# Performance work log

Hardware: AMD Instinct MI355X
Metric: run time of the kernel (lower is better)

## Reference

```python
import jax, jax.numpy as jnp
import numpy as np

N = 50000      # nodes
E = 600000     # edges (avg degree 12)
IN, H, OUT = 128, 256, 256


def setup_inputs() -> dict:
    key = jax.random.key(0)
    ks = jax.random.split(key, 9)
    glorot = lambda k, shp: jax.random.uniform(
        k, shp, jnp.float32, -1.0, 1.0) * np.sqrt(6.0 / (shp[0] + shp[1]))
    return {
        "x": jax.random.normal(ks[0], (N, IN), jnp.float32),
        "src": jax.random.randint(ks[1], (E,), 0, N, jnp.int32),
        "dst": jax.random.randint(ks[2], (E,), 0, N, jnp.int32),
        "W_conv": glorot(ks[3], (IN, H)),
        "b_conv": jnp.zeros((H,), jnp.float32),
        "W_fc": glorot(ks[4], (H, H)),
        "b_fc": jax.random.uniform(ks[5], (H,), jnp.float32, -1, 1) / np.sqrt(H),
        "W_fc2": glorot(ks[6], (H, OUT)),
        "b_fc2": jax.random.uniform(ks[7], (OUT,), jnp.float32, -1, 1) / np.sqrt(OUT),
    }


def reference(x, src, dst, W_conv, b_conv, W_fc, b_fc, W_fc2, b_fc2):
    ones = jnp.ones((E,), x.dtype)
    # dgl GraphConv, norm='both': D_in^{-1/2} A D_out^{-1/2} X W + b
    deg_out = jax.ops.segment_sum(ones, src, num_segments=N)
    deg_in = jax.ops.segment_sum(ones, dst, num_segments=N)
    norm_src = jax.lax.rsqrt(jnp.maximum(deg_out, 1.0))  # [N]
    norm_dst = jax.lax.rsqrt(jnp.maximum(deg_in, 1.0))   # [N]
    feat = x * norm_src[:, None]                          # [N, IN]
    agg = jax.ops.segment_sum(feat[src], dst, num_segments=N)  # gather+scatter SpMM
    h = agg * norm_dst[:, None]
    h = h @ W_conv + b_conv                               # GraphConv weight+bias
    # num_nonl_layers == 2 branch
    h = jax.nn.relu(h) @ W_fc + b_fc
    h = jax.nn.relu(h) @ W_fc2 + b_fc2
    return h
```

## Files before the change

kernel.cpp:

```cpp
#include <hip/hip_runtime.h>

#define NN 50000
#define NE 600000
#define FIN 128
#define CAPS 128
#define CAPU 64
#define PW1 136
#define PW2 264

typedef __attribute__((ext_vector_type(8))) short bf16x8;
typedef __attribute__((ext_vector_type(4))) float f32x4;

__device__ __forceinline__ unsigned short f2bf(float f) {
    union { float f; unsigned int i; } v; v.f = f;
    return (unsigned short)((v.i + 0x7FFFu + ((v.i >> 16) & 1u)) >> 16);
}


__global__ __launch_bounds__(256)
void bin_kernel(const int* __restrict__ src, const int* __restrict__ dst,
                int* __restrict__ cnt_in, int* __restrict__ cnt_out,
                int* __restrict__ csr_src) {
    int e = blockIdx.x * 256 + threadIdx.x;
    if (e < NE) {
        int s = src[e], d = dst[e];
        int p = atomicAdd(&cnt_in[d], 1);
        if (p < CAPU) csr_src[d * CAPS + p] = s;
        atomicAdd(&cnt_out[s], 1);
    }
}

__global__ __launch_bounds__(256)
void gather_kernel(const float* __restrict__ x, const int* __restrict__ csr_src,
                   const int* __restrict__ cnt_in, const int* __restrict__ cnt_out,
                   char* __restrict__ slotbase) {
    int tid  = threadIdx.x;
    int grp  = tid >> 5;
    int lane = tid & 31;
    int r = blockIdx.x * 8 + grp;
    if (r >= NN) return;
    int deg = cnt_in[r];
    float nd = rsqrtf(fmaxf((float)deg, 1.0f));
    int cnt = deg > CAPU ? CAPU : deg;
    const int* bucket = csr_src + (size_t)r * CAPS;
    const float* xb = x + lane * 4;
    float4 acc = {0.f, 0.f, 0.f, 0.f};
    for (int j0 = 0; j0 < cnt; j0 += 32) {
        int c = cnt - j0; if (c > 32) c = 32;
        int sv = 0; float nsl = 0.f;
        if (lane < c) {
            sv  = bucket[j0 + lane];
            nsl = rsqrtf(fmaxf((float)cnt_out[sv], 1.0f));
        }
        int i = 0;
        for (; i + 4 <= c; i += 4) {
            int   s0 = __shfl(sv, i, 32),     s1 = __shfl(sv, i + 1, 32);
            int   s2 = __shfl(sv, i + 2, 32), s3 = __shfl(sv, i + 3, 32);
            float n0 = __shfl(nsl, i, 32),     n1 = __shfl(nsl, i + 1, 32);
            float n2 = __shfl(nsl, i + 2, 32), n3 = __shfl(nsl, i + 3, 32);
            float4 v0 = *(const float4*)(xb + (size_t)s0 * FIN);
            float4 v1 = *(const float4*)(xb + (size_t)s1 * FIN);
            float4 v2 = *(const float4*)(xb + (size_t)s2 * FIN);
            float4 v3 = *(const float4*)(xb + (size_t)s3 * FIN);
            acc.x += v0.x * n0; acc.y += v0.y * n0; acc.z += v0.z * n0; acc.w += v0.w * n0;
            acc.x += v1.x * n1; acc.y += v1.y * n1; acc.z += v1.z * n1; acc.w += v1.w * n1;
            acc.x += v2.x * n2; acc.y += v2.y * n2; acc.z += v2.z * n2; acc.w += v2.w * n2;
            acc.x += v3.x * n3; acc.y += v3.y * n3; acc.z += v3.z * n3; acc.w += v3.w * n3;
        }
        for (; i < c; ++i) {
            int   s  = __shfl(sv,  i, 32);
            float ns = __shfl(nsl, i, 32);
            float4 xv = *(const float4*)(xb + (size_t)s * FIN);
            acc.x += xv.x * ns; acc.y += xv.y * ns;
            acc.z += xv.z * ns; acc.w += xv.w * ns;
        }
    }
    unsigned short o[4];
    o[0] = f2bf(acc.x * nd); o[1] = f2bf(acc.y * nd);
    o[2] = f2bf(acc.z * nd); o[3] = f2bf(acc.w * nd);
    *(uint2*)(slotbase + (size_t)r * 1024 + 768 + lane * 8) = *(const uint2*)o;
}

__global__ __launch_bounds__(256)
void wprep_kernel(const float* __restrict__ Wc, const float* __restrict__ W1,
                  const float* __restrict__ W2, unsigned short* __restrict__ o) {
    int t = blockIdx.x * 256 + threadIdx.x;
    if (t < 32768) {
        int n = t >> 7, k = t & 127;
        o[t] = f2bf(Wc[k * 256 + n]);
    } else if (t < 98304) {
        int i = t - 32768; int n = i >> 8, k = i & 255;
        o[32768 + i] = f2bf(W1[k * 256 + n]);
    } else if (t < 163840) {
        int i = t - 98304; int n = i >> 8, k = i & 255;
        o[98304 + i] = f2bf(W2[k * 256 + n]);
    }
}

__global__ __launch_bounds__(256)
void gemm1_kernel(char* slotbase, const unsigned short* __restrict__ Wct,
                  const float* __restrict__ bc) {
    __shared__ short wsh[64 * PW1];
    int tid = threadIdx.x;
    int wave = tid >> 6, lane = tid & 63;
    int quad = lane >> 4, l16 = lane & 15;
    int m0 = blockIdx.x * 128 + wave * 32;
    bf16x8 a[2][4];
    #pragma unroll
    for (int g = 0; g < 2; ++g) {
        int arow = m0 + g * 16 + l16; if (arow >= NN) arow = NN - 1;
        const unsigned short* Ap =
            (const unsigned short*)(slotbase + (size_t)arow * 1024 + 768) + quad * 8;
        #pragma unroll
        for (int i = 0; i < 4; ++i) a[g][i] = *(const bf16x8*)(Ap + i * 32);
    }
    int sc = tid >> 2, sq = tid & 3;
    #pragma unroll 1
    for (int p = 0; p < 2; ++p) {
        int n0 = blockIdx.y * 128 + p * 64;
        __syncthreads();
        {
            const unsigned short* g = Wct + (size_t)(n0 + sc) * 128 + sq * 32;
            #pragma unroll
            for (int j = 0; j < 4; ++j)
                *(bf16x8*)&wsh[sc * PW1 + sq * 32 + j * 8] = *(const bf16x8*)(g + j * 8);
        }
        __syncthreads();
        f32x4 acc[2][4] = {};
        #pragma unroll
        for (int i = 0; i < 4; ++i) {
            int k0 = i * 32;
            bf16x8 b0 = *(const bf16x8*)&wsh[( 0 + l16) * PW1 + quad * 8 + k0];
            bf16x8 b1 = *(const bf16x8*)&wsh[(16 + l16) * PW1 + quad * 8 + k0];
            bf16x8 b2 = *(const bf16x8*)&wsh[(32 + l16) * PW1 + quad * 8 + k0];
            bf16x8 b3 = *(const bf16x8*)&wsh[(48 + l16) * PW1 + quad * 8 + k0];
            #pragma unroll
            for (int g = 0; g < 2; ++g) {
                acc[g][0] = __builtin_amdgcn_mfma_f32_16x16x32_bf16(a[g][i], b0, acc[g][0], 0, 0, 0);
                acc[g][1] = __builtin_amdgcn_mfma_f32_16x16x32_bf16(a[g][i], b1, acc[g][1], 0, 0, 0);
                acc[g][2] = __builtin_amdgcn_mfma_f32_16x16x32_bf16(a[g][i], b2, acc[g][2], 0, 0, 0);
                acc[g][3] = __builtin_amdgcn_mfma_f32_16x16x32_bf16(a[g][i], b3, acc[g][3], 0, 0, 0);
            }
        }
        #pragma unroll
        for (int c = 0; c < 4; ++c) {
            int col = n0 + c * 16 + l16;
            float bv = bc[col];
            #pragma unroll
            for (int g = 0; g < 2; ++g) {
                #pragma unroll
                for (int r2 = 0; r2 < 4; ++r2) {
                    int rr = m0 + g * 16 + quad * 4 + r2;
                    if (rr < NN)
                        *(unsigned short*)(slotbase + (size_t)rr * 1024 + 2 * col) =
                            f2bf(fmaxf(acc[g][c][r2] + bv, 0.0f));
                }
            }
        }
    }
}

__global__ __launch_bounds__(256)
void gemm2_kernel(char* slotbase, const unsigned short* __restrict__ Wt,
                  const float* __restrict__ bias) {
    __shared__ short wsh[64 * PW2];
    int tid = threadIdx.x;
    int wave = tid >> 6, lane = tid & 63;
    int quad = lane >> 4, l16 = lane & 15;
    int m0 = blockIdx.x * 128 + wave * 32;
    bf16x8 a[2][8];
    #pragma unroll
    for (int g = 0; g < 2; ++g) {
        int arow = m0 + g * 16 + l16; if (arow >= NN) arow = NN - 1;
        const unsigned short* Ap =
            (const unsigned short*)(slotbase + (size_t)arow * 1024) + quad * 8;
        #pragma unroll
        for (int i = 0; i < 8; ++i) a[g][i] = *(const bf16x8*)(Ap + i * 32);
    }
    int sc = tid >> 2, sq = tid & 3;
    #pragma unroll 1
    for (int p = 0; p < 2; ++p) {
        int n0 = blockIdx.y * 128 + p * 64;
        __syncthreads();
        {
            const unsigned short* g = Wt + (size_t)(n0 + sc) * 256 + sq * 64;
            #pragma unroll
            for (int j = 0; j < 8; ++j)
                *(bf16x8*)&wsh[sc * PW2 + sq * 64 + j * 8] = *(const bf16x8*)(g + j * 8);
        }
        __syncthreads();
        f32x4 acc[2][4] = {};
        #pragma unroll
        for (int i = 0; i < 8; ++i) {
            int k0 = i * 32;
            bf16x8 b0 = *(const bf16x8*)&wsh[( 0 + l16) * PW2 + quad * 8 + k0];
            bf16x8 b1 = *(const bf16x8*)&wsh[(16 + l16) * PW2 + quad * 8 + k0];
            bf16x8 b2 = *(const bf16x8*)&wsh[(32 + l16) * PW2 + quad * 8 + k0];
            bf16x8 b3 = *(const bf16x8*)&wsh[(48 + l16) * PW2 + quad * 8 + k0];
            #pragma unroll
            for (int g = 0; g < 2; ++g) {
                acc[g][0] = __builtin_amdgcn_mfma_f32_16x16x32_bf16(a[g][i], b0, acc[g][0], 0, 0, 0);
                acc[g][1] = __builtin_amdgcn_mfma_f32_16x16x32_bf16(a[g][i], b1, acc[g][1], 0, 0, 0);
                acc[g][2] = __builtin_amdgcn_mfma_f32_16x16x32_bf16(a[g][i], b2, acc[g][2], 0, 0, 0);
                acc[g][3] = __builtin_amdgcn_mfma_f32_16x16x32_bf16(a[g][i], b3, acc[g][3], 0, 0, 0);
            }
        }
        #pragma unroll
        for (int c = 0; c < 4; ++c) {
            int col = n0 + c * 16 + l16;
            float bv = bias[col];
            #pragma unroll
            for (int g = 0; g < 2; ++g) {
                #pragma unroll
                for (int r2 = 0; r2 < 4; ++r2) {
                    int rr = m0 + g * 16 + quad * 4 + r2;
                    if (rr < NN)
                        *(unsigned short*)(slotbase + (size_t)rr * 1024 + 512 + 2 * col) =
                            f2bf(fmaxf(acc[g][c][r2] + bv, 0.0f));
                }
            }
        }
    }
}

__global__ __launch_bounds__(256)
void gemm3_kernel(char* slotbase, const unsigned short* __restrict__ Wt,
                  const float* __restrict__ bias) {
    __shared__ short wsh[64 * PW2];
    int tid = threadIdx.x;
    int wave = tid >> 6, lane = tid & 63;
    int quad = lane >> 4, l16 = lane & 15;
    int m0 = blockIdx.x * 64 + wave * 16;
    int arow = m0 + l16; if (arow >= NN) arow = NN - 1;
    const unsigned short* Ap =
        (const unsigned short*)(slotbase + (size_t)arow * 1024 + 512) + quad * 8;
    bf16x8 a[8];
    #pragma unroll
    for (int i = 0; i < 8; ++i) a[i] = *(const bf16x8*)(Ap + i * 32);
    int sc = tid >> 2, sq = tid & 3;
    #pragma unroll 1
    for (int p = 0; p < 4; ++p) {
        __syncthreads();
        {
            const unsigned short* g = Wt + (size_t)(p * 64 + sc) * 256 + sq * 64;
            #pragma unroll
            for (int j = 0; j < 8; ++j)
                *(bf16x8*)&wsh[sc * PW2 + sq * 64 + j * 8] = *(const bf16x8*)(g + j * 8);
        }
        __syncthreads();
        f32x4 ac0 = {0.f,0.f,0.f,0.f}, ac1 = ac0, ac2 = ac0, ac3 = ac0;
        #pragma unroll
        for (int i = 0; i < 8; ++i) {
            int k0 = i * 32;
            bf16x8 b0 = *(const bf16x8*)&wsh[( 0 + l16) * PW2 + quad * 8 + k0];
            bf16x8 b1 = *(const bf16x8*)&wsh[(16 + l16) * PW2 + quad * 8 + k0];
            bf16x8 b2 = *(const bf16x8*)&wsh[(32 + l16) * PW2 + quad * 8 + k0];
            bf16x8 b3 = *(const bf16x8*)&wsh[(48 + l16) * PW2 + quad * 8 + k0];
            ac0 = __builtin_amdgcn_mfma_f32_16x16x32_bf16(a[i], b0, ac0, 0, 0, 0);
            ac1 = __builtin_amdgcn_mfma_f32_16x16x32_bf16(a[i], b1, ac1, 0, 0, 0);
            ac2 = __builtin_amdgcn_mfma_f32_16x16x32_bf16(a[i], b2, ac2, 0, 0, 0);
            ac3 = __builtin_amdgcn_mfma_f32_16x16x32_bf16(a[i], b3, ac3, 0, 0, 0);
        }
        int n0 = p * 64;
        f32x4 accs[4] = {ac0, ac1, ac2, ac3};
        #pragma unroll
        for (int c = 0; c < 4; ++c) {
            int col = n0 + c * 16 + l16;
            float bv = bias[col];
            #pragma unroll
            for (int r2 = 0; r2 < 4; ++r2) {
                int rr = m0 + quad * 4 + r2;
                if (rr < NN)
                    *(float*)(slotbase + (size_t)rr * 1024 + 4 * col) = accs[c][r2] + bv;
            }
        }
    }
}


extern "C" void kernel_launch(void* const* d_in, const int* in_sizes, int n_in,
                              void* d_out, int out_size, void* d_ws, size_t ws_size,
                              hipStream_t stream) {
    const float* x      = (const float*)d_in[0];
    const int*   src    = (const int*)d_in[1];
    const int*   dst    = (const int*)d_in[2];
    const float* W_conv = (const float*)d_in[3];
    const float* b_conv = (const float*)d_in[4];
    const float* W_fc   = (const float*)d_in[5];
    const float* b_fc   = (const float*)d_in[6];
    const float* W_fc2  = (const float*)d_in[7];
    const float* b_fc2  = (const float*)d_in[8];
    char* slotbase = (char*)d_out;

    int* csr_src = (int*)(slotbase + 16000000);

    char* ws = (char*)d_ws;
    int* cnt_out = (int*)(ws + 0);
    int* cnt_in  = (int*)(ws + 204800);
    unsigned short* Wct = (unsigned short*)(ws + 0);
    unsigned short* W1t = (unsigned short*)(ws + 65536);
    unsigned short* W2t = (unsigned short*)(ws + 196608);

    hipMemsetAsync(d_ws, 0, 409600, stream);

    bin_kernel<<<(NE + 255) / 256, 256, 0, stream>>>(src, dst, cnt_in, cnt_out,
                                                     csr_src);
    gather_kernel<<<(NN + 7) / 8, 256, 0, stream>>>(x, csr_src, cnt_in, cnt_out,
                                                    slotbase);
    wprep_kernel<<<640, 256, 0, stream>>>(W_conv, W_fc, W_fc2, (unsigned short*)ws);

    dim3 g12((NN + 127) / 128, 2);
    gemm1_kernel<<<g12, 256, 0, stream>>>(slotbase, Wct, b_conv);
    gemm2_kernel<<<g12, 256, 0, stream>>>(slotbase, W1t, b_fc);
    gemm3_kernel<<<(NN + 63) / 64, 256, 0, stream>>>(slotbase, W2t, b_fc2);
}
```

Before: 271.4 us.

## Pre-scale node features to bf16 before gather, fuse with weight prep

Adds a prep kernel that multiplies each node row by its out-degree norm and stores it as bf16 in workspace. The same launch also converts the weights to bf16. The gather then reads half the bytes per neighbour and skips the per-edge cnt_out lookup and rsqrt. The cost is an extra full pass over x, workspace use, and bf16 rounding of the inputs before accumulation; if the workspace is too small, the old fp32 path is used instead.

Result: faster. 257.0 us (-5.3%).

```diff
diff --git a/kernel.cpp b/kernel.cpp
--- a/kernel.cpp
+++ b/kernel.cpp
@@ -7,6 +7,8 @@
 #define CAPU 64
 #define PW1 136
 #define PW2 264
+#define PRE_BLOCKS 3125
+#define WP_BLOCKS  640
 
 typedef __attribute__((ext_vector_type(8))) short bf16x8;
 typedef __attribute__((ext_vector_type(4))) float f32x4;
@@ -14,6 +16,12 @@
 __device__ __forceinline__ unsigned short f2bf(float f) {
     union { float f; unsigned int i; } v; v.f = f;
     return (unsigned short)((v.i + 0x7FFFu + ((v.i >> 16) & 1u)) >> 16);
+}
+__device__ __forceinline__ float bflo(unsigned int u) {
+    union { unsigned int i; float f; } v; v.i = u << 16; return v.f;
+}
+__device__ __forceinline__ float bfhi(unsigned int u) {
+    union { unsigned int i; float f; } v; v.i = u & 0xffff0000u; return v.f;
 }
 
 
@@ -31,9 +39,87 @@
 }
 
 __global__ __launch_bounds__(256)
-void gather_kernel(const float* __restrict__ x, const int* __restrict__ csr_src,
-                   const int* __restrict__ cnt_in, const int* __restrict__ cnt_out,
+void prep_kernel(const float* __restrict__ x, const int* __restrict__ cnt_out,
+                 unsigned short* __restrict__ xn,
+                 const float* __restrict__ Wc, const float* __restrict__ W1,
+                 const float* __restrict__ W2, unsigned short* __restrict__ wout) {
+    int b = blockIdx.x;
+    if (b < PRE_BLOCKS) {
+        int idx = b * 256 + threadIdx.x;
+        int row = idx >> 4;
+        float sc = rsqrtf(fmaxf((float)cnt_out[row], 1.0f));
+        const float4* xp = (const float4*)(x + (size_t)idx * 8);
+        float4 a = xp[0], c = xp[1];
+        unsigned int w0 = f2bf(a.x * sc) | ((unsigned int)f2bf(a.y * sc) << 16);
+        unsigned int w1 = f2bf(a.z * sc) | ((unsigned int)f2bf(a.w * sc) << 16);
+        unsigned int w2 = f2bf(c.x * sc) | ((unsigned int)f2bf(c.y * sc) << 16);
+        unsigned int w3 = f2bf(c.z * sc) | ((unsigned int)f2bf(c.w * sc) << 16);
+        uint4 o = {w0, w1, w2, w3};
+        *(uint4*)(xn + (size_t)idx * 8) = o;
+    } else {
+        int t = (b - PRE_BLOCKS) * 256 + threadIdx.x;
+        if (t < 32768) {
+            int n = t >> 7, k = t & 127;
+            wout[t] = f2bf(Wc[k * 256 + n]);
+        } else if (t < 98304) {
+            int i = t - 32768; int n = i >> 8, k = i & 255;
+            wout[32768 + i] = f2bf(W1[k * 256 + n]);
+        } else if (t < 163840) {
+            int i = t - 98304; int n = i >> 8, k = i & 255;
+            wout[98304 + i] = f2bf(W2[k * 256 + n]);
+        }
+    }
+}
+
+__global__ __launch_bounds__(256)
+void gather_kernel(const unsigned short* __restrict__ xn,
+                   const int* __restrict__ csr_src,
+                   const int* __restrict__ cnt_in,
                    char* __restrict__ slotbase) {
+    int tid  = threadIdx.x;
+    int grp  = tid >> 5;
+    int lane = tid & 31;
+    int r = blockIdx.x * 8 + grp;
+    if (r >= NN) return;
+    int deg = cnt_in[r];
+    float nd = rsqrtf(fmaxf((float)deg, 1.0f));
+    int cnt = deg > CAPU ? CAPU : deg;
+    const int* bucket = csr_src + (size_t)r * CAPS;
+    const unsigned short* xb = xn + lane * 4;
+    float4 acc = {0.f, 0.f, 0.f, 0.f};
+    for (int j0 = 0; j0 < cnt; j0 += 32) {
+        int c = cnt - j0; if (c > 32) c = 32;
+        int sv = (lane < c) ? bucket[j0 + lane] : 0;
+        int i = 0;
+        for (; i + 4 <= c; i += 4) {
+            int s0 = __shfl(sv, i,     32), s1 = __shfl(sv, i + 1, 32);
+            int s2 = __shfl(sv, i + 2, 32), s3 = __shfl(sv, i + 3, 32);
+            uint2 w0 = *(const uint2*)(xb + (size_t)s0 * FIN);
+            uint2 w1 = *(const uint2*)(xb + (size_t)s1 * FIN);
+            uint2 w2 = *(const uint2*)(xb + (size_t)s2 * FIN);
+            uint2 w3 = *(const uint2*)(xb + (size_t)s3 * FIN);
+            acc.x += bflo(w0.x); acc.y += bfhi(w0.x); acc.z += bflo(w0.y); acc.w += bfhi(w0.y);
+            acc.x += bflo(w1.x); acc.y += bfhi(w1.x); acc.z += bflo(w1.y); acc.w += bfhi(w1.y);
+            acc.x += bflo(w2.x); acc.y += bfhi(w2.x); acc.z += bflo(w2.y); acc.w += bfhi(w2.y);
+            acc.x += bflo(w3.x); acc.y += bfhi(w3.x); acc.z += bflo(w3.y); acc.w += bfhi(w3.y);
+        }
+        for (; i < c; ++i) {
+            int s = __shfl(sv, i, 32);
+            uint2 w = *(const uint2*)(xb + (size_t)s * FIN);
+            acc.x += bflo(w.x); acc.y += bfhi(w.x);
+            acc.z += bflo(w.y); acc.w += bfhi(w.y);
+        }
+    }
+    unsigned short o[4];
+    o[0] = f2bf(acc.x * nd); o[1] = f2bf(acc.y * nd);
+    o[2] = f2bf(acc.z * nd); o[3] = f2bf(acc.w * nd);
+    *(uint2*)(slotbase + (size_t)r * 1024 + 768 + lane * 8) = *(const uint2*)o;
+}
+
+__global__ __launch_bounds__(256)
+void gather_fb_kernel(const float* __restrict__ x, const int* __restrict__ csr_src,
+                      const int* __restrict__ cnt_in, const int* __restrict__ cnt_out,
+                      char* __restrict__ slotbase) {
     int tid  = threadIdx.x;
     int grp  = tid >> 5;
     int lane = tid & 31;
@@ -52,22 +138,7 @@
             sv  = bucket[j0 + lane];
             nsl = rsqrtf(fmaxf((float)cnt_out[sv], 1.0f));
         }
-        int i = 0;
-        for (; i + 4 <= c; i += 4) {
-            int   s0 = __shfl(sv, i, 32),     s1 = __shfl(sv, i + 1, 32);
-            int   s2 = __shfl(sv, i + 2, 32), s3 = __shfl(sv, i + 3, 32);
-            float n0 = __shfl(nsl, i, 32),     n1 = __shfl(nsl, i + 1, 32);
-            float n2 = __shfl(nsl, i + 2, 32), n3 = __shfl(nsl, i + 3, 32);
-            float4 v0 = *(const float4*)(xb + (size_t)s0 * FIN);
-            float4 v1 = *(const float4*)(xb + (size_t)s1 * FIN);
-            float4 v2 = *(const float4*)(xb + (size_t)s2 * FIN);
-            float4 v3 = *(const float4*)(xb + (size_t)s3 * FIN);
-            acc.x += v0.x * n0; acc.y += v0.y * n0; acc.z += v0.z * n0; acc.w += v0.w * n0;
-            acc.x += v1.x * n1; acc.y += v1.y * n1; acc.z += v1.z * n1; acc.w += v1.w * n1;
-            acc.x += v2.x * n2; acc.y += v2.y * n2; acc.z += v2.z * n2; acc.w += v2.w * n2;
-            acc.x += v3.x * n3; acc.y += v3.y * n3; acc.z += v3.z * n3; acc.w += v3.w * n3;
-        }
-        for (; i < c; ++i) {
+        for (int i = 0; i < c; ++i) {
             int   s  = __shfl(sv,  i, 32);
             float ns = __shfl(nsl, i, 32);
             float4 xv = *(const float4*)(xb + (size_t)s * FIN);
@@ -297,20 +368,34 @@
     char* ws = (char*)d_ws;
     int* cnt_out = (int*)(ws + 0);
     int* cnt_in  = (int*)(ws + 204800);
-    unsigned short* Wct = (unsigned short*)(ws + 0);
-    unsigned short* W1t = (unsigned short*)(ws + 65536);
-    unsigned short* W2t = (unsigned short*)(ws + 196608);
 
     hipMemsetAsync(d_ws, 0, 409600, stream);
 
     bin_kernel<<<(NE + 255) / 256, 256, 0, stream>>>(src, dst, cnt_in, cnt_out,
                                                      csr_src);
-    gather_kernel<<<(NN + 7) / 8, 256, 0, stream>>>(x, csr_src, cnt_in, cnt_out,
-                                                    slotbase);
-    wprep_kernel<<<640, 256, 0, stream>>>(W_conv, W_fc, W_fc2, (unsigned short*)ws);
 
     dim3 g12((NN + 127) / 128, 2);
-    gemm1_kernel<<<g12, 256, 0, stream>>>(slotbase, Wct, b_conv);
-    gemm2_kernel<<<g12, 256, 0, stream>>>(slotbase, W1t, b_fc);
-    gemm3_kernel<<<(NN + 63) / 64, 256, 0, stream>>>(slotbase, W2t, b_fc2);
-}
+    if (ws_size >= 13537408) {
+        unsigned short* xn  = (unsigned short*)(ws + 409728);
+        unsigned short* Wct = (unsigned short*)(ws + 13209728);
+        unsigned short* W1t = Wct + 32768;
+        unsigned short* W2t = Wct + 98304;
+        prep_kernel<<<PRE_BLOCKS + WP_BLOCKS, 256, 0, stream>>>(
+            x, cnt_out, xn, W_conv, W_fc, W_fc2, Wct);
+        gather_kernel<<<(NN + 7) / 8, 256, 0, stream>>>(xn, csr_src, cnt_in,
+                                                        slotbase);
+        gemm1_kernel<<<g12, 256, 0, stream>>>(slotbase, Wct, b_conv);
+        gemm2_kernel<<<g12, 256, 0, stream>>>(slotbase, W1t, b_fc);
+        gemm3_kernel<<<(NN + 63) / 64, 256, 0, stream>>>(slotbase, W2t, b_fc2);
+    } else {
+        unsigned short* Wct = (unsigned short*)(ws + 0);
+        unsigned short* W1t = Wct + 32768;
+        unsigned short* W2t = Wct + 98304;
+        gather_fb_kernel<<<(NN + 7) / 8, 256, 0, stream>>>(x, csr_src, cnt_in,
+                                                           cnt_out, slotbase);
+        wprep_kernel<<<WP_BLOCKS, 256, 0, stream>>>(W_conv, W_fc, W_fc2, Wct);
+        gemm1_kernel<<<g12, 256, 0, stream>>>(slotbase, Wct, b_conv);
+        gemm2_kernel<<<g12, 256, 0, stream>>>(slotbase, W1t, b_fc);
+        gemm3_kernel<<<(NN + 63) / 64, 256, 0, stream>>>(slotbase, W2t, b_fc2);
+    }
+}
```
